# Kernel tuning notes

Measured on AMD Instinct MI355X. Metric: run time of the kernel, lower is better.

Reference implementation:

```python
import jax, jax.numpy as jnp
import numpy as np
from jax import lax

DN = ('NCHW', 'OIHW', 'NCHW')

def _conv(x, w, pad):
    return lax.conv_general_dilated(x, w, (1, 1), pad, dimension_numbers=DN)

def _bn(x, p, eps=1e-5):
    # p: [4, C] rows = gamma, beta, mean, var ; inference-mode batchnorm
    g, b, m, v = p[0], p[1], p[2], p[3]
    scale = g / jnp.sqrt(v + eps)
    return (x - m[:, None, None]) * scale[:, None, None] + b[:, None, None]

def setup_inputs() -> dict:
    key = jax.random.key(0)
    ks = jax.random.split(key, 12)
    B, C, H, W = 16, 512, 56, 56
    mid = C // 2
    def bn_params(k):
        k1, k2, k3, k4 = jax.random.split(k, 4)
        g = 1.0 + 0.1 * jax.random.normal(k1, (mid,), jnp.float32)
        b = 0.1 * jax.random.normal(k2, (mid,), jnp.float32)
        m = 0.1 * jax.random.normal(k3, (mid,), jnp.float32)
        v = 0.5 + jax.random.uniform(k4, (mid,), jnp.float32)
        return jnp.stack([g, b, m, v])
    return {
        'x': jax.random.normal(ks[0], (B, C, H, W), jnp.float32),
        'w_main': 0.03 * jax.random.normal(ks[1], (mid, C, 3, 3), jnp.float32),
        'w_1x1': 0.05 * jax.random.normal(ks[2], (mid, C, 1, 1), jnp.float32),
        'w31': 0.05 * jax.random.normal(ks[3], (mid, C, 1, 1), jnp.float32),
        'bn31': bn_params(ks[4]),
        'w33': 0.05 * jax.random.normal(ks[5], (mid, mid, 3, 3), jnp.float32),
        'bn33': bn_params(ks[6]),
        'wa1': 0.05 * jax.random.normal(ks[7], (mid, C, 1, 1), jnp.float32),
        'bna1': bn_params(ks[8]),
        'bna2': bn_params(ks[9]),
        'fuse_weight': jnp.ones((4,), jnp.float32),
        'c_score': jax.random.normal(ks[10], (2 * C,), jnp.float32),
    }

def reference(x, w_main, w_1x1, w31, bn31, w33, bn33, wa1, bna1, bna2, fuse_weight, c_score):
    c = x.shape[1]
    # four branches (note: forward applies BN only inside the 3x3 and avg branches)
    acs_main = _conv(x * fuse_weight[0], w_main, 'SAME')
    acs_1x1 = _conv(x * fuse_weight[1], w_1x1, 'VALID')
    acs_3x3 = _bn(_conv(_bn(_conv(x * fuse_weight[2], w31, 'VALID'), bn31), w33, 'SAME'), bn33)
    avg_in = _bn(_conv(x * fuse_weight[3], wa1, 'VALID'), bna1)
    # AvgPool2d(k=3, s=1, p=1, count_include_pad=True)
    pooled = lax.reduce_window(avg_in, 0.0, lax.add, (1, 1, 3, 3), (1, 1, 1, 1),
                               [(0, 0), (0, 0), (1, 1), (1, 1)]) / 9.0
    acs_avg = _bn(pooled, bna2)
    out = jnp.concatenate([acs_main, acs_1x1, acs_3x3, acs_avg], axis=1)  # [B, 2c, H, W]
    # sparse 1x1 selection: output channel i = input channel ind[i] * sigmoid(c_score[ind[i]])
    _, ind = lax.top_k(c_score, c)
    scale = jax.nn.sigmoid(c_score)[ind]  # [c]
    out = out[:, ind] * scale[None, :, None, None]
    return out
```

## Files before the change

### kernel.cpp

```cpp
#include <hip/hip_runtime.h>
#include <hip/hip_bf16.h>
#include <cstdint>
#include <cstddef>

typedef _Float16 f16x8_t __attribute__((ext_vector_type(8)));
typedef float    f32x4_t __attribute__((ext_vector_type(4)));
typedef unsigned short u16x8_t __attribute__((ext_vector_type(8)));
typedef unsigned short u16x4_t __attribute__((ext_vector_type(4)));

__device__ __forceinline__ unsigned short f2h(float f) {
    return __builtin_bit_cast(unsigned short, (_Float16)f);
}
__device__ __forceinline__ float h2f(unsigned short h) {
    return (float)__builtin_bit_cast(_Float16, h);
}
__device__ __forceinline__ f16x8_t load_h8(const unsigned short* p) {
    u16x8_t r = *(const u16x8_t*)p;
    return __builtin_bit_cast(f16x8_t, r);
}

#define BATCH 16
#define CFULL 512
#define CMID  256
#define HW    3136
#define WDIM  56

#define PLANE_SH 2784
#define LDS_SHORTS (4 * 2784)

__global__ void prep_tabs(const float* __restrict__ cscore,
                          const float* __restrict__ bn31, const float* __restrict__ bn33,
                          const float* __restrict__ bna1, const float* __restrict__ bna2,
                          int* __restrict__ pos_tab, float* __restrict__ scale_tab,
                          float* __restrict__ bnab)
{
    __shared__ float s[1024];
    int t = threadIdx.x;
    s[t] = cscore[t];
    __syncthreads();
    float sj = s[t];
    int cnt = 0;
    for (int k = 0; k < 1024; ++k) {
        float sk = s[k];
        cnt += (sk > sj) || (sk == sj && k < t);
    }
    pos_tab[t]   = (cnt < 512) ? cnt : -1;
    scale_tab[t] = 1.0f / (1.0f + expf(-sj));

    if (t < 256) {
        const float* srcs[4] = {bn31, bn33, bna1, bna2};
        #pragma unroll
        for (int q = 0; q < 4; ++q) {
            const float* sp = srcs[q];
            float g = sp[t], b = sp[256 + t], m = sp[512 + t], v = sp[768 + t];
            float a = g * rsqrtf(v + 1e-5f);
            bnab[q * 512 + t]       = a;
            bnab[q * 512 + 256 + t] = b - m * a;
        }
    }
}

__global__ void prep_weights(const float* __restrict__ w_main, const float* __restrict__ w_1x1,
                             const float* __restrict__ w31, const float* __restrict__ wa1,
                             const float* __restrict__ w33, const float* __restrict__ fw,
                             unsigned short* __restrict__ Wcat,
                             unsigned short* __restrict__ Wmain,
                             unsigned short* __restrict__ W33r)
{
    int i = blockIdx.x * 256 + threadIdx.x;
    if (i < 393216) {
        int row = i >> 9, c = i & 511;
        float v;
        if (row < 256)      v = w_1x1[row * 512 + c] * fw[1];
        else if (row < 512) v = w31[(row - 256) * 512 + c] * fw[2];
        else                v = wa1[(row - 512) * 512 + c] * fw[3];
        Wcat[((c >> 5) * 768 + row) * 32 + (c & 31)] = f2h(v);
    } else if (i < 393216 + 1179648) {
        int j = i - 393216;
        int o = j / 4608, r = j % 4608, tap = r >> 9, c = r & 511;
        Wmain[(((c >> 5) * 9 + tap) * 256 + o) * 32 + (c & 31)] =
            f2h(w_main[(size_t)(o * 512 + c) * 9 + tap] * fw[0]);
    } else if (i < 2162688) {
        int j = i - 1572864;
        int o = j / 2304, r = j % 2304, tap = r >> 8, c = r & 255;
        W33r[(((c >> 5) * 9 + tap) * 256 + o) * 32 + (c & 31)] =
            f2h(w33[(size_t)(o * 256 + c) * 9 + tap]);
    }
}

__global__ void transpose_x(const float* __restrict__ x, unsigned short* __restrict__ xt)
{
    __shared__ unsigned short tile[64][65];
    int t = threadIdx.x;
    int hw0 = blockIdx.x * 64, c0 = blockIdx.y * 64, b = blockIdx.z;
    const float* xb = x + ((size_t)b * CFULL + c0) * HW + hw0;
    int hwL = t & 63, cL = t >> 6;
    #pragma unroll
    for (int i = 0; i < 16; ++i) {
        int c = cL + i * 4;
        tile[c][hwL] = f2h(xb[(size_t)c * HW + hwL]);
    }
    __syncthreads();
    int c8 = (t & 7) * 8, hw = t >> 3;
    #pragma unroll
    for (int i = 0; i < 2; ++i) {
        int hh = hw + i * 32;
        u16x8_t v;
        #pragma unroll
        for (int j = 0; j < 8; ++j) v[j] = tile[c8 + j][hh];
        *(u16x8_t*)(xt + ((size_t)b * HW + hw0 + hh) * CFULL + c0 + c8) = v;
    }
}

template<int CIN, int NTAP, int MODE>
__device__ __forceinline__ void conv_body(
    const unsigned short* __restrict__ X,
    const unsigned short* __restrict__ Wr,
    float* __restrict__ out,
    unsigned short* __restrict__ u_dst,
    unsigned short* __restrict__ avg_dst,
    const float* __restrict__ bnab,
    const int* __restrict__ pos_tab,
    const float* __restrict__ scale_tab,
    unsigned short* smem, int b, int ob, int pb)
{
    const int t    = threadIdx.x;
    const int lane = t & 63;
    const int wid  = t >> 6;
    const int wm = wid >> 1, wn = wid & 1;
    const int lr = lane & 15;
    const int ko = (lane >> 4) * 8;
    const int kqp = (lane >> 4) * PLANE_SH;
    const int row0 = pb * 4;

    const int o_wave = ob * 128 + wm * 64;
    const int p_wave = pb * 224 + wn * 112;

    int bofs[7];
    #pragma unroll
    for (int n = 0; n < 7; ++n) {
        int p = p_wave + n * 16 + lr;
        bofs[n] = kqp + ((p / WDIM - row0) * 58 + p % WDIM) * 8;
    }

    const int r_lo = (NTAP == 9) ? 0 : 1;
    const int nitems = ((NTAP == 9) ? 6 : 4) * 224;
    int  s_src[6];
    int  s_dst[6];
    bool s_val[6];
    #pragma unroll
    for (int i = 0; i < 6; ++i) {
        int idx = t + i * 256;
        bool act = idx < nitems;
        int r   = r_lo + idx / 224;
        int rm  = idx % 224;
        int col = rm >> 2, sub = rm & 3;
        int ir  = row0 + r - 1;
        s_val[i] = act && ((unsigned)ir < (unsigned)WDIM);
        s_src[i] = (ir * WDIM + col) * CIN + sub * 8;
        s_dst[i] = sub * PLANE_SH + (r * 58 + col + 1) * 8;
    }

    #pragma unroll
    for (int i = 0; i < 7; ++i) {
        int j = t + i * 256;
        if (j < LDS_SHORTS / 8)
            *(u16x8_t*)(smem + j * 8) = (u16x8_t){0, 0, 0, 0, 0, 0, 0, 0};
    }

    f32x4_t acc[4][7];
    #pragma unroll
    for (int m = 0; m < 4; ++m)
        #pragma unroll
        for (int n = 0; n < 7; ++n)
            acc[m][n] = (f32x4_t){0.f, 0.f, 0.f, 0.f};

    const int astep = (MODE == 1) ? 768 * 32 : 256 * 32;
    const unsigned short* am[4];
    #pragma unroll
    for (int m = 0; m < 4; ++m)
        am[m] = Wr + (size_t)(o_wave + m * 16 + lr) * 32 + ko;

    const unsigned short* xb = X + (size_t)b * HW * CIN;
    const int KCH = CIN / 32;

    for (int kch = 0; kch < KCH; ++kch) {
        __syncthreads();
        u16x8_t buf[6];
        #pragma unroll
        for (int i = 0; i < 6; ++i)
            if (s_val[i]) buf[i] = *(const u16x8_t*)(xb + s_src[i] + kch * 32);
        #pragma unroll
        for (int i = 0; i < 6; ++i)
            if (s_val[i]) *(u16x8_t*)(smem + s_dst[i]) = buf[i];
        __syncthreads();

        #pragma unroll
        for (int tap = 0; tap < NTAP; ++tap) {
            const int toff = (NTAP == 9) ? (((tap / 3) * 58 + tap % 3) * 8)
                                         : (59 * 8);
            f16x8_t af[4];
            #pragma unroll
            for (int m = 0; m < 4; ++m)
                af[m] = load_h8(am[m] + (size_t)(kch * NTAP + tap) * astep);
            f16x8_t bf[7];
            #pragma unroll
            for (int n = 0; n < 7; ++n)
                bf[n] = load_h8(smem + bofs[n] + toff);
            __builtin_amdgcn_s_setprio(1);
            #pragma unroll
            for (int m = 0; m < 4; ++m)
                #pragma unroll
                for (int n = 0; n < 7; ++n)
                    acc[m][n] = __builtin_amdgcn_mfma_f32_16x16x32_f16(af[m], bf[n], acc[m][n], 0, 0, 0);
            __builtin_amdgcn_s_setprio(0);
        }
    }

    const int fq = lane >> 4;
    const int seg = (MODE == 1) ? (ob >> 1) : 0;
    const bool bn_write = (MODE == 1) && (seg != 0);

    #pragma unroll
    for (int m = 0; m < 4; ++m) {
        const int orow = o_wave + m * 16 + fq * 4;
        #pragma unroll
        for (int n = 0; n < 7; ++n) {
            const int p = p_wave + n * 16 + lr;
            f32x4_t v = acc[m][n];
            if (bn_write) {
                const int lc0 = orow - seg * 256;
                const float* ab = (seg == 1) ? (bnab + 0 * 512) : (bnab + 2 * 512);
                unsigned short* dst = (seg == 1) ? u_dst : avg_dst;
                u16x4_t pk;
                #pragma unroll
                for (int j = 0; j < 4; ++j) {
                    float a = ab[lc0 + j], bb = ab[256 + lc0 + j];
                    pk[j] = f2h(a * v[j] + bb);
                }
                *(u16x4_t*)(dst + ((size_t)b * HW + p) * CMID + lc0) = pk;
            } else {
                const int cbase = (MODE == 0) ? 0 : ((MODE == 2) ? 512 : 256);
                #pragma unroll
                for (int j = 0; j < 4; ++j) {
                    int o = orow + j;
                    float val2 = v[j];
                    if (MODE == 2) val2 = bnab[512 + o] * val2 + bnab[512 + 256 + o];
                    int jc = cbase + o;
                    int pos = pos_tab[jc];
                    if (pos >= 0)
                        out[((size_t)b * CFULL + pos) * HW + p] = val2 * scale_tab[jc];
                }
            }
        }
    }
}

template<int CIN, int MODE>
__device__ __forceinline__ void conv_sched(
    const unsigned short* __restrict__ X,
    const unsigned short* __restrict__ Wr,
    float* __restrict__ out,
    const float* __restrict__ bnab,
    const int* __restrict__ pos_tab,
    const float* __restrict__ scale_tab,
    unsigned short* smem, int b, int ob, int pb)
{
    const int t    = threadIdx.x;
    const int lane = t & 63;
    const int wid  = t >> 6;
    const int wm = wid >> 1, wn = wid & 1;
    const int lr = lane & 15;
    const int ko = (lane >> 4) * 8;
    const int kqp = (lane >> 4) * PLANE_SH;
    const int row0 = pb * 4;

    const int o_wave = ob * 128 + wm * 64;
    const int p_wave = pb * 224 + wn * 112;

    int bofs[7];
    #pragma unroll
    for (int n = 0; n < 7; ++n) {
        int p = p_wave + n * 16 + lr;
        bofs[n] = kqp + ((p / WDIM - row0) * 58 + p % WDIM) * 8;
    }

    const int nitems = 6 * 224;
    const int dump_off = 2 * LDS_SHORTS + (t & 63) * 8 + (wid & 3) * 512;
    int s_src[6];
    int s_dst[6];
    #pragma unroll
    for (int i = 0; i < 6; ++i) {
        int idx = t + i * 256;
        int r   = idx / 224;
        int rm  = idx % 224;
        int col = rm >> 2, sub = rm & 3;
        int ir  = row0 + r - 1;
        bool v  = (idx < nitems) && ((unsigned)ir < (unsigned)WDIM);
        int ir_c = v ? ir : 0;
        s_src[i] = (ir_c * WDIM + col) * CIN + sub * 8;
        s_dst[i] = v ? (sub * PLANE_SH + (r * 58 + col + 1) * 8) : dump_off;
    }

    #pragma unroll
    for (int i = 0; i < 14; ++i) {
        int j = t + i * 256;
        if (j < 2 * LDS_SHORTS / 8)
            *(u16x8_t*)(smem + j * 8) = (u16x8_t){0, 0, 0, 0, 0, 0, 0, 0};
    }

    f32x4_t acc[4][7];
    #pragma unroll
    for (int m = 0; m < 4; ++m)
        #pragma unroll
        for (int n = 0; n < 7; ++n)
            acc[m][n] = (f32x4_t){0.f, 0.f, 0.f, 0.f};

    const int astep = 256 * 32;
    const unsigned short* am[4];
    #pragma unroll
    for (int m = 0; m < 4; ++m)
        am[m] = Wr + (size_t)(o_wave + m * 16 + lr) * 32 + ko;

    const unsigned short* xb = X + (size_t)b * HW * CIN;
    const int KCH = CIN / 32;
    const int NT = KCH * 9;

    f16x8_t af[3][4];

    u16x8_t sbuf[6];
    __syncthreads();
    #pragma unroll
    for (int i = 0; i < 6; ++i)
        sbuf[i] = *(const u16x8_t*)(xb + s_src[i]);
    asm volatile("s_waitcnt vmcnt(0)" ::: "memory");
    #pragma unroll
    for (int i = 0; i < 6; ++i)
        *(u16x8_t*)(smem + s_dst[i]) = sbuf[i];
    #pragma unroll
    for (int m = 0; m < 4; ++m)
        af[0][m] = load_h8(am[m]);
    #pragma unroll
    for (int m = 0; m < 4; ++m)
        af[1][m] = load_h8(am[m] + (size_t)1 * astep);
    asm volatile("s_waitcnt lgkmcnt(0)" ::: "memory");
    __builtin_amdgcn_s_barrier();

    #pragma unroll 1
    for (int kch = 0; kch < KCH; ++kch) {
        const unsigned short* rbuf = smem + (kch & 1) * LDS_SHORTS;
        unsigned short* wbuf = smem + ((kch + 1) & 1) * LDS_SHORTS;
        const int nk = (kch + 1 < KCH) ? (kch + 1) : 0;

        #pragma unroll
        for (int tap = 0; tap < 9; ++tap) {
            const int fill = (tap + 2) % 3;
            const int use  = tap % 3;
            int kt = kch * 9 + tap + 2;
            if (kt >= NT) kt -= NT;
            #pragma unroll
            for (int m = 0; m < 4; ++m)
                af[fill][m] = load_h8(am[m] + (size_t)kt * astep);
            if (tap == 7) {
                #pragma unroll
                for (int i = 0; i < 6; ++i)
                    sbuf[i] = *(const u16x8_t*)(xb + s_src[i] + nk * 32);
            }
            const int toff = ((tap / 3) * 58 + tap % 3) * 8;
            f16x8_t bf[7];
            #pragma unroll
            for (int n = 0; n < 7; ++n)
                bf[n] = load_h8(rbuf + bofs[n] + toff);
            if (tap < 7)
                asm volatile("s_waitcnt vmcnt(8) lgkmcnt(0)" ::: "memory");
            else
                asm volatile("s_waitcnt vmcnt(14) lgkmcnt(0)" ::: "memory");
            __builtin_amdgcn_sched_barrier(0);
            __builtin_amdgcn_s_setprio(1);
            #pragma unroll
            for (int m = 0; m < 4; ++m)
                #pragma unroll
                for (int n = 0; n < 7; ++n)
                    acc[m][n] = __builtin_amdgcn_mfma_f32_16x16x32_f16(af[use][m], bf[n], acc[m][n], 0, 0, 0);
            __builtin_amdgcn_s_setprio(0);
            __builtin_amdgcn_sched_barrier(0);
        }

        asm volatile("s_waitcnt vmcnt(4)" ::: "memory");
        #pragma unroll
        for (int i = 0; i < 6; ++i)
            *(u16x8_t*)(wbuf + s_dst[i]) = sbuf[i];
        asm volatile("s_waitcnt lgkmcnt(0)" ::: "memory");
        __builtin_amdgcn_s_barrier();
    }

    const int fq = lane >> 4;
    #pragma unroll
    for (int m = 0; m < 4; ++m) {
        const int orow = o_wave + m * 16 + fq * 4;
        #pragma unroll
        for (int n = 0; n < 7; ++n) {
            const int p = p_wave + n * 16 + lr;
            f32x4_t v = acc[m][n];
            const int cbase = (MODE == 0) ? 0 : 512;
            #pragma unroll
            for (int j = 0; j < 4; ++j) {
                int o = orow + j;
                float val2 = v[j];
                if (MODE == 2) val2 = bnab[512 + o] * val2 + bnab[512 + 256 + o];
                int jc = cbase + o;
                int pos = pos_tab[jc];
                if (pos >= 0)
                    out[((size_t)b * CFULL + pos) * HW + p] = val2 * scale_tab[jc];
            }
        }
    }
}

__global__ __launch_bounds__(256, 2)
void fusedK(const unsigned short* __restrict__ X,
            const unsigned short* __restrict__ Wcat,
            float* __restrict__ out,
            unsigned short* __restrict__ u_dst,
            unsigned short* __restrict__ avg_dst,
            const float* __restrict__ bnab,
            const int* __restrict__ pos_tab,
            const float* __restrict__ scale_tab)
{
    __shared__ unsigned short smem[LDS_SHORTS];
    const int id = blockIdx.x;
    const int xcd = id & 7, slot = id >> 3;
    const int b = xcd + 8 * (slot / 84);
    const int u = slot % 84;
    conv_body<512, 1, 1>(X, Wcat, out, u_dst, avg_dst, bnab,
                         pos_tab, scale_tab, smem, b, u / 14, u % 14);
}

__global__ __launch_bounds__(256, 2)
void longK(const unsigned short* __restrict__ X,
           const unsigned short* __restrict__ Wmain,
           const unsigned short* __restrict__ U,
           const unsigned short* __restrict__ W33r,
           const unsigned short* __restrict__ avgin,
           float* __restrict__ out,
           const float* __restrict__ bnab,
           const int* __restrict__ pos_tab,
           const float* __restrict__ scale_tab)
{
    __shared__ unsigned short smem[2 * LDS_SHORTS + 2048];
    const int id = blockIdx.x;
    const int xcd = id & 7, slot = id >> 3;
    if (slot < 112) {
        const int b = xcd + 8 * (slot / 56);
        const int rr = slot % 56;
        const int idx = rr >> 1;
        const int ob = idx / 14, pb = idx % 14;
        if ((rr & 1) == 0)
            conv_sched<512, 0>(X, Wmain, out, bnab, pos_tab, scale_tab, smem, b, ob, pb);
        else
            conv_sched<256, 2>(U, W33r, out, bnab, pos_tab, scale_tab, smem, b, ob, pb);
    } else {
        const int s2 = slot - 112;
        const int b = xcd + 8 * (s2 / 392);
        const int q = s2 % 392;
        const int t = threadIdx.x;
        const int p = q * 8 + (t >> 5);
        const int c0 = (t & 31) * 8;
        const int h = p / WDIM, w = p % WDIM;
        const float* ab2 = bnab + 3 * 512;
        float s[8];
        #pragma unroll
        for (int j = 0; j < 8; ++j) s[j] = 0.f;
        #pragma unroll
        for (int dh = -1; dh <= 1; ++dh) {
            int hh = h + dh;
            if ((unsigned)hh >= (unsigned)WDIM) continue;
            #pragma unroll
            for (int dw = -1; dw <= 1; ++dw) {
                int ww = w + dw;
                if ((unsigned)ww >= (unsigned)WDIM) continue;
                u16x8_t v = *(const u16x8_t*)(avgin + ((size_t)b * HW + hh * WDIM + ww) * CMID + c0);
                #pragma unroll
                for (int j = 0; j < 8; ++j) s[j] += h2f(v[j]);
            }
        }
        #pragma unroll
        for (int j = 0; j < 8; ++j) {
            int c = c0 + j;
            int jc = 768 + c;
            int pos = pos_tab[jc];
            if (pos >= 0) {
                float val = (s[j] * (1.f / 9.f)) * ab2[c] + ab2[256 + c];
                out[((size_t)b * CFULL + pos) * HW + p] = val * scale_tab[jc];
            }
        }
    }
}

extern "C" void kernel_launch(void* const* d_in, const int* in_sizes, int n_in,
                              void* d_out, int out_size, void* d_ws, size_t ws_size,
                              hipStream_t stream) {
    (void)in_sizes; (void)n_in; (void)out_size; (void)ws_size;
    const float* x      = (const float*)d_in[0];
    const float* w_main = (const float*)d_in[1];
    const float* w_1x1  = (const float*)d_in[2];
    const float* w31    = (const float*)d_in[3];
    const float* bn31   = (const float*)d_in[4];
    const float* w33    = (const float*)d_in[5];
    const float* bn33   = (const float*)d_in[6];
    const float* wa1    = (const float*)d_in[7];
    const float* bna1   = (const float*)d_in[8];
    const float* bna2   = (const float*)d_in[9];
    const float* fw     = (const float*)d_in[10];
    const float* cscore = (const float*)d_in[11];
    float* out = (float*)d_out;

    char* ws = (char*)d_ws;
    unsigned short* x_nhwc = (unsigned short*)(ws);
    unsigned short* u_nhwc = (unsigned short*)(ws + 51380224);
    unsigned short* avgin  = (unsigned short*)(ws + 77070336);
    unsigned short* Wcat   = (unsigned short*)(ws + 102760448);
    unsigned short* Wmain  = (unsigned short*)(ws + 103546880);
    unsigned short* W33r   = (unsigned short*)(ws + 105906176);
    float*          bnab   = (float*)        (ws + 107085824);
    int*            pos_tab= (int*)          (ws + 107094016);
    float*          scl_tab= (float*)        (ws + 107098112);

    dim3 blk(256);

    prep_tabs<<<dim3(1), dim3(1024), 0, stream>>>(cscore, bn31, bn33, bna1, bna2,
                                                  pos_tab, scl_tab, bnab);
    prep_weights<<<dim3(8448), blk, 0, stream>>>(w_main, w_1x1, w31, wa1, w33, fw,
                                                 Wcat, Wmain, W33r);
    transpose_x<<<dim3(49, 8, 16), blk, 0, stream>>>(x, x_nhwc);

    fusedK<<<dim3(1344), blk, 0, stream>>>(x_nhwc, Wcat, out,
                                           u_nhwc, avgin, bnab, pos_tab, scl_tab);

    longK<<<dim3(7168), blk, 0, stream>>>(x_nhwc, Wmain, u_nhwc, W33r, avgin,
                                          out, bnab, pos_tab, scl_tab);
}
```

Baseline: 421.0 us.

## Rebalance conv work across two kernels and make avg-pool separable via LDS

Moves half of the 3x3 main-conv tiles (batches 0-7) into the first kernel next to the 1x1 fused convs, so both launches carry more even work. The avg-pool branch now processes one image row per block: a vertical 3-tap sum goes into LDS in fp16, then a horizontal 3-tap sum is read from LDS, cutting global loads from 9 to 3 per output. This trades a larger LDS footprint in the first kernel and an extra fp16 rounding of the partial sums for less global traffic and a better load balance.

```diff
diff --git a/kernel.cpp b/kernel.cpp
--- a/kernel.cpp
+++ b/kernel.cpp
@@ -418,7 +418,8 @@
 }
 
 __global__ __launch_bounds__(256, 2)
-void fusedK(const unsigned short* __restrict__ X,
+void convK1(const unsigned short* __restrict__ X,
+            const unsigned short* __restrict__ Wmain,
             const unsigned short* __restrict__ Wcat,
             float* __restrict__ out,
             unsigned short* __restrict__ u_dst,
@@ -427,71 +428,99 @@
             const int* __restrict__ pos_tab,
             const float* __restrict__ scale_tab)
 {
-    __shared__ unsigned short smem[LDS_SHORTS];
-    const int id = blockIdx.x;
-    const int xcd = id & 7, slot = id >> 3;
-    const int b = xcd + 8 * (slot / 84);
-    const int u = slot % 84;
-    conv_body<512, 1, 1>(X, Wcat, out, u_dst, avg_dst, bnab,
-                         pos_tab, scale_tab, smem, b, u / 14, u % 14);
-}
-
-__global__ __launch_bounds__(256, 2)
-void longK(const unsigned short* __restrict__ X,
-           const unsigned short* __restrict__ Wmain,
-           const unsigned short* __restrict__ U,
-           const unsigned short* __restrict__ W33r,
-           const unsigned short* __restrict__ avgin,
-           float* __restrict__ out,
-           const float* __restrict__ bnab,
-           const int* __restrict__ pos_tab,
-           const float* __restrict__ scale_tab)
-{
     __shared__ unsigned short smem[2 * LDS_SHORTS + 2048];
     const int id = blockIdx.x;
     const int xcd = id & 7, slot = id >> 3;
-    if (slot < 112) {
-        const int b = xcd + 8 * (slot / 56);
-        const int rr = slot % 56;
-        const int idx = rr >> 1;
-        const int ob = idx / 14, pb = idx % 14;
-        if ((rr & 1) == 0)
-            conv_sched<512, 0>(X, Wmain, out, bnab, pos_tab, scale_tab, smem, b, ob, pb);
+    if (slot < 28) {
+        conv_sched<512, 0>(X, Wmain, out, bnab, pos_tab, scale_tab,
+                           smem, xcd, slot / 14, slot % 14);
+    } else {
+        const int g = slot - 28;
+        const int b = xcd + 8 * (g / 84);
+        const int u = g % 84;
+        conv_body<512, 1, 1>(X, Wcat, out, u_dst, avg_dst, bnab,
+                             pos_tab, scale_tab, smem, b, u / 14, u % 14);
+    }
+}
+
+__global__ __launch_bounds__(256, 2)
+void convK2(const unsigned short* __restrict__ X,
+            const unsigned short* __restrict__ Wmain,
+            const unsigned short* __restrict__ U,
+            const unsigned short* __restrict__ W33r,
+            const unsigned short* __restrict__ avgin,
+            float* __restrict__ out,
+            const float* __restrict__ bnab,
+            const int* __restrict__ pos_tab,
+            const float* __restrict__ scale_tab)
+{
+    __shared__ unsigned short smem[2 * LDS_SHORTS + 2048];
+    const int id = blockIdx.x;
+    const int xcd = id & 7, slot = id >> 3;
+    if (slot < 84) {
+        const int m = slot / 3, r = slot % 3;
+        const int ob = m / 14, pb = m % 14;
+        if (r == 0)
+            conv_sched<512, 0>(X, Wmain, out, bnab, pos_tab, scale_tab,
+                               smem, 8 + xcd, ob, pb);
         else
-            conv_sched<256, 2>(U, W33r, out, bnab, pos_tab, scale_tab, smem, b, ob, pb);
+            conv_sched<256, 2>(U, W33r, out, bnab, pos_tab, scale_tab,
+                               smem, (r == 1) ? xcd : (xcd + 8), ob, pb);
     } else {
-        const int s2 = slot - 112;
-        const int b = xcd + 8 * (s2 / 392);
-        const int q = s2 % 392;
+        const int q = slot - 84;
+        const int b = xcd + 8 * (q / 56);
+        const int h = q % 56;
         const int t = threadIdx.x;
-        const int p = q * 8 + (t >> 5);
         const int c0 = (t & 31) * 8;
-        const int h = p / WDIM, w = p % WDIM;
+        const int ws = t >> 5;
         const float* ab2 = bnab + 3 * 512;
-        float s[8];
-        #pragma unroll
-        for (int j = 0; j < 8; ++j) s[j] = 0.f;
-        #pragma unroll
-        for (int dh = -1; dh <= 1; ++dh) {
-            int hh = h + dh;
-            if ((unsigned)hh >= (unsigned)WDIM) continue;
+        const unsigned short* ab_base = avgin + (size_t)b * HW * CMID;
+
+        #pragma unroll
+        for (int i = 0; i < 7; ++i) {
+            int w = ws * 7 + i;
+            float s[8];
+            #pragma unroll
+            for (int j = 0; j < 8; ++j) s[j] = 0.f;
+            #pragma unroll
+            for (int dh = -1; dh <= 1; ++dh) {
+                int hh = h + dh;
+                if ((unsigned)hh >= (unsigned)WDIM) continue;
+                u16x8_t v = *(const u16x8_t*)(ab_base + (size_t)(hh * WDIM + w) * CMID + c0);
+                #pragma unroll
+                for (int j = 0; j < 8; ++j) s[j] += h2f(v[j]);
+            }
+            u16x8_t pk;
+            #pragma unroll
+            for (int j = 0; j < 8; ++j) pk[j] = f2h(s[j]);
+            *(u16x8_t*)(smem + w * CMID + c0) = pk;
+        }
+        __syncthreads();
+
+        #pragma unroll
+        for (int i = 0; i < 7; ++i) {
+            int w = ws * 7 + i;
+            float s[8];
+            #pragma unroll
+            for (int j = 0; j < 8; ++j) s[j] = 0.f;
             #pragma unroll
             for (int dw = -1; dw <= 1; ++dw) {
                 int ww = w + dw;
                 if ((unsigned)ww >= (unsigned)WDIM) continue;
-                u16x8_t v = *(const u16x8_t*)(avgin + ((size_t)b * HW + hh * WDIM + ww) * CMID + c0);
+                u16x8_t v = *(const u16x8_t*)(smem + ww * CMID + c0);
                 #pragma unroll
                 for (int j = 0; j < 8; ++j) s[j] += h2f(v[j]);
             }
-        }
-        #pragma unroll
-        for (int j = 0; j < 8; ++j) {
-            int c = c0 + j;
-            int jc = 768 + c;
-            int pos = pos_tab[jc];
-            if (pos >= 0) {
-                float val = (s[j] * (1.f / 9.f)) * ab2[c] + ab2[256 + c];
-                out[((size_t)b * CFULL + pos) * HW + p] = val * scale_tab[jc];
+            const int p = h * WDIM + w;
+            #pragma unroll
+            for (int j = 0; j < 8; ++j) {
+                int c = c0 + j;
+                int jc = 768 + c;
+                int pos = pos_tab[jc];
+                if (pos >= 0) {
+                    float val = (s[j] * (1.f / 9.f)) * ab2[c] + ab2[256 + c];
+                    out[((size_t)b * CFULL + pos) * HW + p] = val * scale_tab[jc];
+                }
             }
         }
     }
@@ -534,9 +563,9 @@
                                                  Wcat, Wmain, W33r);
     transpose_x<<<dim3(49, 8, 16), blk, 0, stream>>>(x, x_nhwc);
 
-    fusedK<<<dim3(1344), blk, 0, stream>>>(x_nhwc, Wcat, out,
+    convK1<<<dim3(1568), blk, 0, stream>>>(x_nhwc, Wmain, Wcat, out,
                                            u_nhwc, avgin, bnab, pos_tab, scl_tab);
 
-    longK<<<dim3(7168), blk, 0, stream>>>(x_nhwc, Wmain, u_nhwc, W33r, avgin,
-                                          out, bnab, pos_tab, scl_tab);
-}
+    convK2<<<dim3(1568), blk, 0, stream>>>(x_nhwc, Wmain, u_nhwc, W33r, avgin,
+                                           out, bnab, pos_tab, scl_tab);
+}
```

Result: faster. 387.4 us (median of 3 runs) (-8.0%).
